# Optimization experiments

Measured on AMD Instinct MI355X. Metric: run time of the kernel, lower is better.

## Reference

```python
import math
import jax, jax.numpy as jnp
import numpy as np

DIM = 2048
N_HEADS = 16
HEAD_DIM = DIM // N_HEADS  # 128
BSZ = 2
SEQLEN = 2048
ROPE_THETA = 500000.0


def _make_freqs(seqlen, head_dim, theta):
    inv = 1.0 / (theta ** (np.arange(0, head_dim, 2, dtype=np.float32) / head_dim))
    t = np.arange(seqlen, dtype=np.float32)
    f = np.outer(t, inv)  # [S, hd//2]
    return jnp.asarray(np.cos(f)), jnp.asarray(np.sin(f))


def setup_inputs() -> dict:
    key = jax.random.key(0)
    kx, kq, kk, kv, ko = jax.random.split(key, 5)
    scale = 0.02
    x = jax.random.normal(kx, (BSZ, SEQLEN, DIM), dtype=jnp.float32)
    wq = jax.random.normal(kq, (DIM, DIM), dtype=jnp.float32) * scale
    wk = jax.random.normal(kk, (DIM, DIM), dtype=jnp.float32) * scale
    wv = jax.random.normal(kv, (DIM, DIM), dtype=jnp.float32) * scale
    wo = jax.random.normal(ko, (DIM, DIM), dtype=jnp.float32) * scale
    freqs_cos, freqs_sin = _make_freqs(SEQLEN, HEAD_DIM, ROPE_THETA)
    # causal additive mask: 0 on/below diag, -inf above
    mask = jnp.triu(jnp.full((SEQLEN, SEQLEN), float('-inf'), dtype=jnp.float32), k=1)
    return {"x": x, "start_pos": 0, "freqs_cos": freqs_cos, "freqs_sin": freqs_sin,
            "mask": mask, "wq": wq, "wk": wk, "wv": wv, "wo": wo}


def _apply_rope(t, cos, sin):
    # t: [B, S, H, hd]; cos/sin: [S, hd//2]
    b, s, h, hd = t.shape
    tr = t.reshape(b, s, h, hd // 2, 2)
    a, bb = tr[..., 0], tr[..., 1]
    c = cos[None, :, None, :]
    sn = sin[None, :, None, :]
    out_r = a * c - bb * sn
    out_i = a * sn + bb * c
    return jnp.stack([out_r, out_i], axis=-1).reshape(b, s, h, hd)


def reference(x, start_pos, freqs_cos, freqs_sin, mask, wq, wk, wv, wo):
    b, s, _ = x.shape
    xq = (x @ wq.T).reshape(b, s, N_HEADS, HEAD_DIM)
    xk = (x @ wk.T).reshape(b, s, N_HEADS, HEAD_DIM)
    xv = (x @ wv.T).reshape(b, s, N_HEADS, HEAD_DIM)
    xq = _apply_rope(xq, freqs_cos, freqs_sin)
    xk = _apply_rope(xk, freqs_cos, freqs_sin)
    # [B, H, S, hd]
    xq = xq.transpose(0, 2, 1, 3)
    xk = xk.transpose(0, 2, 1, 3)
    xv = xv.transpose(0, 2, 1, 3)
    scores = jnp.einsum('bhqd,bhkd->bhqk', xq, xk) / math.sqrt(HEAD_DIM)
    scores = scores + mask[None, None, :, :]
    probs = jax.nn.softmax(scores.astype(jnp.float32), axis=-1).astype(xq.dtype)
    out = jnp.einsum('bhqk,bhkd->bhqd', probs, xv)
    out = out.transpose(0, 2, 1, 3).reshape(b, s, -1)
    return out @ wo.T
```

## Files before the change

kernel.cpp:

```cpp
#include <hip/hip_runtime.h>
#include <stdint.h>

#define DIM 2048
#define SEQ 2048
#define NHEADS 16
#define HDIM 128
#define BSZ 2
#define ROWS (BSZ*SEQ)

typedef uint16_t u16;
typedef __attribute__((ext_vector_type(8))) short bf16x8;
typedef __attribute__((ext_vector_type(4))) float fx4;
typedef __attribute__((ext_vector_type(4))) uint16_t u16x4;

typedef const __attribute__((address_space(1))) uint32_t* gp_t;
typedef __attribute__((address_space(3))) uint32_t* lp_t;
#define GLL16(g, l) __builtin_amdgcn_global_load_lds((gp_t)(g), (lp_t)(l), 16, 0, 0)

__device__ inline u16 f2bf(float f) {
  union { float f; uint32_t u; } v; v.f = f;
  uint32_t u = v.u;
  u += 0x7FFFu + ((u >> 16) & 1u);
  return (u16)(u >> 16);
}
__device__ inline float bf2f(u16 h) {
  union { uint32_t u; float f; } v; v.u = ((uint32_t)h) << 16;
  return v.f;
}

__global__ __launch_bounds__(256) void cvt_kernel(const float* __restrict__ src,
                                                  u16* __restrict__ dst, int n4) {
  int i = blockIdx.x * 256 + threadIdx.x;
  if (i >= n4) return;
  fx4 f = *(const fx4*)(src + (size_t)i * 4);
  u16x4 o;
  o[0] = f2bf(f[0]); o[1] = f2bf(f[1]); o[2] = f2bf(f[2]); o[3] = f2bf(f[3]);
  *(u16x4*)(dst + (size_t)i * 4) = o;
}

__device__ inline void gemm128_core(const u16* __restrict__ A, const u16* __restrict__ B,
                                    u16 (&As)[128][32], u16 (&Bs)[128][32],
                                    fx4 (&acc)[4][4], int M0, int N0) {
  const int tid  = threadIdx.x;
  const int lane = tid & 63;
  const int wave = tid >> 6;
  const int wm = (wave >> 1) * 64;
  const int wn = (wave & 1) * 64;
  const int l16 = lane & 15;
  const int q8  = (lane >> 4) * 8;
#pragma unroll
  for (int tm = 0; tm < 4; ++tm)
#pragma unroll
    for (int tn = 0; tn < 4; ++tn) acc[tm][tn] = fx4{0.f, 0.f, 0.f, 0.f};

  const int wrow = wave * 32;
  const size_t laneA = (size_t)(M0 + wrow + (lane >> 2)) * DIM + (lane & 3) * 8;
  const size_t laneB = (size_t)(N0 + wrow + (lane >> 2)) * DIM + (lane & 3) * 8;

  for (int k0 = 0; k0 < DIM; k0 += 32) {
    __syncthreads();
    GLL16(A + laneA + k0,            &As[wrow][0]);
    GLL16(A + laneA + 16 * DIM + k0, &As[wrow + 16][0]);
    GLL16(B + laneB + k0,            &Bs[wrow][0]);
    GLL16(B + laneB + 16 * DIM + k0, &Bs[wrow + 16][0]);
    __syncthreads();
    bf16x8 af[4], bfr[4];
#pragma unroll
    for (int t = 0; t < 4; ++t) {
      af[t]  = *(const bf16x8*)&As[wm + t * 16 + l16][q8];
      bfr[t] = *(const bf16x8*)&Bs[wn + t * 16 + l16][q8];
    }
#pragma unroll
    for (int tm = 0; tm < 4; ++tm)
#pragma unroll
      for (int tn = 0; tn < 4; ++tn)
        acc[tm][tn] = __builtin_amdgcn_mfma_f32_16x16x32_bf16(af[tm], bfr[tn], acc[tm][tn], 0, 0, 0);
  }
}

__global__ __launch_bounds__(256) void gemm_qkv(const u16* __restrict__ A,
    const u16* __restrict__ B0, const u16* __restrict__ B1, const u16* __restrict__ B2,
    u16* __restrict__ C0, u16* __restrict__ C1, u16* __restrict__ C2) {
  __shared__ __align__(16) u16 As[128][32];
  __shared__ __align__(16) u16 Bs[128][32];
  const u16* B = (blockIdx.z == 0) ? B0 : (blockIdx.z == 1) ? B1 : B2;
  u16* C       = (blockIdx.z == 0) ? C0 : (blockIdx.z == 1) ? C1 : C2;
  const int M0 = blockIdx.y * 128, N0 = blockIdx.x * 128;
  fx4 acc[4][4];
  gemm128_core(A, B, As, Bs, acc, M0, N0);
  const int lane = threadIdx.x & 63, wave = threadIdx.x >> 6;
  const int wm = (wave >> 1) * 64, wn = (wave & 1) * 64;
  const int l16 = lane & 15, quad = lane >> 4;
#pragma unroll
  for (int tm = 0; tm < 4; ++tm)
#pragma unroll
    for (int tn = 0; tn < 4; ++tn)
#pragma unroll
      for (int r = 0; r < 4; ++r) {
        size_t row = (size_t)(M0 + wm + tm * 16 + quad * 4 + r);
        size_t col = (size_t)(N0 + wn + tn * 16 + l16);
        C[row * DIM + col] = f2bf(acc[tm][tn][r]);
      }
}

__global__ __launch_bounds__(256) void gemm_out(const u16* __restrict__ A,
                                                const u16* __restrict__ B,
                                                float* __restrict__ C) {
  __shared__ __align__(16) u16 As[128][32];
  __shared__ __align__(16) u16 Bs[128][32];
  const int M0 = blockIdx.y * 128, N0 = blockIdx.x * 128;
  fx4 acc[4][4];
  gemm128_core(A, B, As, Bs, acc, M0, N0);
  const int lane = threadIdx.x & 63, wave = threadIdx.x >> 6;
  const int wm = (wave >> 1) * 64, wn = (wave & 1) * 64;
  const int l16 = lane & 15, quad = lane >> 4;
#pragma unroll
  for (int tm = 0; tm < 4; ++tm)
#pragma unroll
    for (int tn = 0; tn < 4; ++tn)
#pragma unroll
      for (int r = 0; r < 4; ++r) {
        size_t row = (size_t)(M0 + wm + tm * 16 + quad * 4 + r);
        size_t col = (size_t)(N0 + wn + tn * 16 + l16);
        C[row * DIM + col] = acc[tm][tn][r];
      }
}

__global__ __launch_bounds__(256) void rope_kernel(u16* __restrict__ q, u16* __restrict__ k,
                                                   const float* __restrict__ fcos,
                                                   const float* __restrict__ fsin) {
  int idx = blockIdx.x * 256 + threadIdx.x;
  int t = idx >> 22;
  int p_all = idx & ((1 << 22) - 1);
  u16* ptr = t ? k : q;
  int row = p_all >> 10;
  int r   = p_all & 1023;
  int h   = r >> 6;
  int p   = r & 63;
  int s   = row & (SEQ - 1);
  size_t base = (size_t)row * DIM + h * HDIM + 2 * p;
  float a = bf2f(ptr[base]), b = bf2f(ptr[base + 1]);
  float c = fcos[s * 64 + p], sn = fsin[s * 64 + p];
  ptr[base]     = f2bf(a * c - b * sn);
  ptr[base + 1] = f2bf(a * sn + b * c);
}

__global__ __launch_bounds__(256) void vtrans_kernel(const u16* __restrict__ v,
                                                     u16* __restrict__ vtg) {
  __shared__ __align__(16) u16 T[128][72];
  const int tid = threadIdx.x;
  const int s0 = blockIdx.x * 64;
  const int bh = blockIdx.y;
  const int b = bh >> 4, h = bh & 15;
  const size_t vb = ((size_t)b * SEQ + s0) * DIM + h * HDIM;
#pragma unroll
  for (int i = 0; i < 4; ++i) {
    int c = i * 256 + tid;
    int s = c >> 4;
    int d0 = (c & 15) * 8;
    bf16x8 x = *(const bf16x8*)(v + vb + (size_t)s * DIM + d0);
#pragma unroll
    for (int j = 0; j < 8; ++j) T[d0 + j][s] = (u16)x[j];
  }
  __syncthreads();
  const size_t ob = ((size_t)bh * HDIM) * SEQ + s0;
#pragma unroll
  for (int i = 0; i < 4; ++i) {
    int c = i * 256 + tid;
    int d = c >> 3;
    int s8 = (c & 7) * 8;
    *(bf16x8*)(vtg + ob + (size_t)d * SEQ + s8) = *(const bf16x8*)&T[d][s8];
  }
}

__global__ __launch_bounds__(256) void attn_kernel(const u16* __restrict__ qm,
                                                   const u16* __restrict__ km,
                                                   const u16* __restrict__ vtg,
                                                   u16* __restrict__ ao) {
  __shared__ __align__(16) u16 Ks[64][136];
  __shared__ __align__(16) u16 Vt[128][72];
  __shared__ __align__(16) u16 Ps[4][16][72];
  const int tid = threadIdx.x;
  const int lane = tid & 63, wave = tid >> 6;
  const int l16 = lane & 15, quad = lane >> 4;
  const int bh = blockIdx.x;
  const int qt = (SEQ / 64 - 1) - blockIdx.y;
  const int b = bh >> 4, h = bh & 15;
  const int q0 = qt * 64;
  const size_t brow = (size_t)b * SEQ;
  const int hc = h * HDIM;
  const size_t vbase = (size_t)bh * HDIM * SEQ;

  bf16x8 aq[4];
  {
    size_t qbase = (brow + q0 + wave * 16 + l16) * DIM + hc;
#pragma unroll
    for (int dc = 0; dc < 4; ++dc)
      aq[dc] = *(const bf16x8*)(qm + qbase + dc * 32 + quad * 8);
  }
  fx4 o[8];
#pragma unroll
  for (int i = 0; i < 8; ++i) o[i] = fx4{0.f, 0.f, 0.f, 0.f};
  float mr[4], lr[4];
#pragma unroll
  for (int r = 0; r < 4; ++r) { mr[r] = -3e38f; lr[r] = 0.f; }

  bf16x8 kreg[4], vreg[4];
#pragma unroll
  for (int i = 0; i < 4; ++i) {
    int c = i * 256 + tid;
    kreg[i] = *(const bf16x8*)(km + (brow + (c >> 4)) * DIM + hc + (c & 15) * 8);
    vreg[i] = *(const bf16x8*)(vtg + vbase + (size_t)(c >> 3) * SEQ + (c & 7) * 8);
  }

  for (int kt = 0; kt <= qt; ++kt) {
    __syncthreads();
#pragma unroll
    for (int i = 0; i < 4; ++i) {
      int c = i * 256 + tid;
      *(bf16x8*)&Ks[c >> 4][(c & 15) * 8] = kreg[i];
      *(bf16x8*)&Vt[c >> 3][(c & 7) * 8] = vreg[i];
    }
    __syncthreads();
    if (kt < qt) {
      const int kv1 = (kt + 1) * 64;
#pragma unroll
      for (int i = 0; i < 4; ++i) {
        int c = i * 256 + tid;
        kreg[i] = *(const bf16x8*)(km + (brow + kv1 + (c >> 4)) * DIM + hc + (c & 15) * 8);
        vreg[i] = *(const bf16x8*)(vtg + vbase + (size_t)(c >> 3) * SEQ + kv1 + (c & 7) * 8);
      }
    }
    fx4 s[4];
#pragma unroll
    for (int tn = 0; tn < 4; ++tn) {
      fx4 acc = fx4{0.f, 0.f, 0.f, 0.f};
#pragma unroll
      for (int dc = 0; dc < 4; ++dc) {
        bf16x8 bk = *(const bf16x8*)&Ks[tn * 16 + l16][dc * 32 + quad * 8];
        acc = __builtin_amdgcn_mfma_f32_16x16x32_bf16(aq[dc], bk, acc, 0, 0, 0);
      }
      s[tn] = acc * 0.08838834764831845f;
    }
    if (kt == qt) {
      const int kv0 = kt * 64;
#pragma unroll
      for (int tn = 0; tn < 4; ++tn) {
        int kvpos = kv0 + tn * 16 + l16;
#pragma unroll
        for (int r = 0; r < 4; ++r) {
          int qpos = q0 + wave * 16 + quad * 4 + r;
          if (kvpos > qpos) s[tn][r] = -1e30f;
        }
      }
    }
    float alpha[4];
#pragma unroll
    for (int r = 0; r < 4; ++r) {
      float t = fmaxf(fmaxf(s[0][r], s[1][r]), fmaxf(s[2][r], s[3][r]));
      t = fmaxf(t, __shfl_xor(t, 1));
      t = fmaxf(t, __shfl_xor(t, 2));
      t = fmaxf(t, __shfl_xor(t, 4));
      t = fmaxf(t, __shfl_xor(t, 8));
      float mnew = fmaxf(mr[r], t);
      alpha[r] = __expf(mr[r] - mnew);
      float sm = 0.f;
#pragma unroll
      for (int tn = 0; tn < 4; ++tn) {
        float p = __expf(s[tn][r] - mnew);
        s[tn][r] = p;
        sm += p;
      }
      sm += __shfl_xor(sm, 1);
      sm += __shfl_xor(sm, 2);
      sm += __shfl_xor(sm, 4);
      sm += __shfl_xor(sm, 8);
      lr[r] = lr[r] * alpha[r] + sm;
      mr[r] = mnew;
    }
#pragma unroll
    for (int tn = 0; tn < 4; ++tn)
#pragma unroll
      for (int r = 0; r < 4; ++r)
        Ps[wave][quad * 4 + r][tn * 16 + l16] = f2bf(s[tn][r]);
#pragma unroll
    for (int nt = 0; nt < 8; ++nt) {
      fx4 t = o[nt];
      t[0] *= alpha[0]; t[1] *= alpha[1]; t[2] *= alpha[2]; t[3] *= alpha[3];
      o[nt] = t;
    }
#pragma unroll
    for (int t2 = 0; t2 < 2; ++t2) {
      bf16x8 ap = *(const bf16x8*)&Ps[wave][l16][t2 * 32 + quad * 8];
#pragma unroll
      for (int nt = 0; nt < 8; ++nt) {
        bf16x8 bv = *(const bf16x8*)&Vt[nt * 16 + l16][t2 * 32 + quad * 8];
        o[nt] = __builtin_amdgcn_mfma_f32_16x16x32_bf16(ap, bv, o[nt], 0, 0, 0);
      }
    }
  }
#pragma unroll
  for (int nt = 0; nt < 8; ++nt)
#pragma unroll
    for (int r = 0; r < 4; ++r) {
      float val = o[nt][r] / lr[r];
      size_t row = brow + q0 + wave * 16 + quad * 4 + r;
      ao[row * DIM + hc + nt * 16 + l16] = f2bf(val);
    }
}

extern "C" void kernel_launch(void* const* d_in, const int* in_sizes, int n_in,
                              void* d_out, int out_size, void* d_ws, size_t ws_size,
                              hipStream_t stream) {
  const float* x    = (const float*)d_in[0];
  const float* fcos = (const float*)d_in[2];
  const float* fsin = (const float*)d_in[3];
  const float* wq   = (const float*)d_in[5];
  const float* wk   = (const float*)d_in[6];
  const float* wv   = (const float*)d_in[7];
  const float* wo   = (const float*)d_in[8];
  float* out = (float*)d_out;

  const size_t XN = (size_t)ROWS * DIM;
  const size_t WN = (size_t)DIM * DIM;
  u16* ws  = (u16*)d_ws;
  u16* xb  = ws;
  u16* wqb = xb + XN;
  u16* wkb = wqb + WN;
  u16* wvb = wkb + WN;
  u16* wob = wvb + WN;
  u16* q   = wob + WN;
  u16* k   = q + XN;
  u16* v   = k + XN;
  u16* ao  = v + XN;
  u16* vtg = xb;

  cvt_kernel<<<(int)(XN / 4 / 256), 256, 0, stream>>>(x, xb, (int)(XN / 4));
  cvt_kernel<<<(int)(WN / 4 / 256), 256, 0, stream>>>(wq, wqb, (int)(WN / 4));
  cvt_kernel<<<(int)(WN / 4 / 256), 256, 0, stream>>>(wk, wkb, (int)(WN / 4));
  cvt_kernel<<<(int)(WN / 4 / 256), 256, 0, stream>>>(wv, wvb, (int)(WN / 4));
  cvt_kernel<<<(int)(WN / 4 / 256), 256, 0, stream>>>(wo, wob, (int)(WN / 4));

  gemm_qkv<<<dim3(DIM / 128, ROWS / 128, 3), 256, 0, stream>>>(xb, wqb, wkb, wvb, q, k, v);

  rope_kernel<<<2 * ROWS * 1024 / 256, 256, 0, stream>>>(q, k, fcos, fsin);
  vtrans_kernel<<<dim3(SEQ / 64, BSZ * NHEADS), 256, 0, stream>>>(v, vtg);

  attn_kernel<<<dim3(BSZ * NHEADS, SEQ / 64), 256, 0, stream>>>(q, k, vtg, ao);

  gemm_out<<<dim3(DIM / 128, ROWS / 128), 256, 0, stream>>>(ao, wob, out);
}
```

Baseline: 461.8 us.

## Fuse conversions, fold RoPE into QKV GEMM epilogue, enlarge attention query tile

Result: slower. 483.0 us (+4.6%).

```diff
diff --git a/kernel.cpp b/kernel.cpp
--- a/kernel.cpp
+++ b/kernel.cpp
@@ -28,11 +28,23 @@
   return v.f;
 }
 
-__global__ __launch_bounds__(256) void cvt_kernel(const float* __restrict__ src,
-                                                  u16* __restrict__ dst, int n4) {
+__global__ __launch_bounds__(256) void cvt5_kernel(const float* __restrict__ sx,
+    const float* __restrict__ s1, const float* __restrict__ s2,
+    const float* __restrict__ s3, const float* __restrict__ s4,
+    u16* __restrict__ dst) {
+  const int XC = (ROWS * DIM) / 4;
+  const int WC = (DIM * DIM) / 4;
   int i = blockIdx.x * 256 + threadIdx.x;
-  if (i >= n4) return;
-  fx4 f = *(const fx4*)(src + (size_t)i * 4);
+  const float* src;
+  int off;
+  if (i < XC) { src = sx; off = i; }
+  else {
+    int t = i - XC;
+    int w = t >> 20;
+    off = t & (WC - 1);
+    src = (w == 0) ? s1 : (w == 1) ? s2 : (w == 2) ? s3 : s4;
+  }
+  fx4 f = *(const fx4*)(src + (size_t)off * 4);
   u16x4 o;
   o[0] = f2bf(f[0]); o[1] = f2bf(f[1]); o[2] = f2bf(f[2]); o[3] = f2bf(f[3]);
   *(u16x4*)(dst + (size_t)i * 4) = o;
@@ -80,7 +92,8 @@
 
 __global__ __launch_bounds__(256) void gemm_qkv(const u16* __restrict__ A,
     const u16* __restrict__ B0, const u16* __restrict__ B1, const u16* __restrict__ B2,
-    u16* __restrict__ C0, u16* __restrict__ C1, u16* __restrict__ C2) {
+    u16* __restrict__ C0, u16* __restrict__ C1, u16* __restrict__ C2,
+    const float* __restrict__ fcos, const float* __restrict__ fsin) {
   __shared__ __align__(16) u16 As[128][32];
   __shared__ __align__(16) u16 Bs[128][32];
   const u16* B = (blockIdx.z == 0) ? B0 : (blockIdx.z == 1) ? B1 : B2;
@@ -91,16 +104,39 @@
   const int lane = threadIdx.x & 63, wave = threadIdx.x >> 6;
   const int wm = (wave >> 1) * 64, wn = (wave & 1) * 64;
   const int l16 = lane & 15, quad = lane >> 4;
-#pragma unroll
-  for (int tm = 0; tm < 4; ++tm)
-#pragma unroll
-    for (int tn = 0; tn < 4; ++tn)
-#pragma unroll
-      for (int r = 0; r < 4; ++r) {
-        size_t row = (size_t)(M0 + wm + tm * 16 + quad * 4 + r);
-        size_t col = (size_t)(N0 + wn + tn * 16 + l16);
-        C[row * DIM + col] = f2bf(acc[tm][tn][r]);
-      }
+  if (blockIdx.z < 2) {
+    const bool odd = l16 & 1;
+#pragma unroll
+    for (int tm = 0; tm < 4; ++tm)
+#pragma unroll
+      for (int tn = 0; tn < 4; ++tn) {
+        int col = N0 + wn + tn * 16 + l16;
+        int p = (col & 127) >> 1;
+#pragma unroll
+        for (int r = 0; r < 4; ++r) {
+          int row = M0 + wm + tm * 16 + quad * 4 + r;
+          int s_pos = row & (SEQ - 1);
+          float val = acc[tm][tn][r];
+          float partner = __shfl_xor(val, 1);
+          float c = fcos[s_pos * 64 + p], sn = fsin[s_pos * 64 + p];
+          float a = odd ? partner : val;
+          float bb = odd ? val : partner;
+          float outv = odd ? (a * sn + bb * c) : (a * c - bb * sn);
+          C[(size_t)row * DIM + col] = f2bf(outv);
+        }
+      }
+  } else {
+#pragma unroll
+    for (int tm = 0; tm < 4; ++tm)
+#pragma unroll
+      for (int tn = 0; tn < 4; ++tn)
+#pragma unroll
+        for (int r = 0; r < 4; ++r) {
+          size_t row = (size_t)(M0 + wm + tm * 16 + quad * 4 + r);
+          size_t col = (size_t)(N0 + wn + tn * 16 + l16);
+          C[row * DIM + col] = f2bf(acc[tm][tn][r]);
+        }
+  }
 }
 
 __global__ __launch_bounds__(256) void gemm_out(const u16* __restrict__ A,
@@ -126,25 +162,6 @@
       }
 }
 
-__global__ __launch_bounds__(256) void rope_kernel(u16* __restrict__ q, u16* __restrict__ k,
-                                                   const float* __restrict__ fcos,
-                                                   const float* __restrict__ fsin) {
-  int idx = blockIdx.x * 256 + threadIdx.x;
-  int t = idx >> 22;
-  int p_all = idx & ((1 << 22) - 1);
-  u16* ptr = t ? k : q;
-  int row = p_all >> 10;
-  int r   = p_all & 1023;
-  int h   = r >> 6;
-  int p   = r & 63;
-  int s   = row & (SEQ - 1);
-  size_t base = (size_t)row * DIM + h * HDIM + 2 * p;
-  float a = bf2f(ptr[base]), b = bf2f(ptr[base + 1]);
-  float c = fcos[s * 64 + p], sn = fsin[s * 64 + p];
-  ptr[base]     = f2bf(a * c - b * sn);
-  ptr[base + 1] = f2bf(a * sn + b * c);
-}
-
 __global__ __launch_bounds__(256) void vtrans_kernel(const u16* __restrict__ v,
                                                      u16* __restrict__ vtg) {
   __shared__ __align__(16) u16 T[128][72];
@@ -173,37 +190,43 @@
   }
 }
 
-__global__ __launch_bounds__(256) void attn_kernel(const u16* __restrict__ qm,
-                                                   const u16* __restrict__ km,
-                                                   const u16* __restrict__ vtg,
-                                                   u16* __restrict__ ao) {
+__global__ __launch_bounds__(256, 2) void attn_kernel(const u16* __restrict__ qm,
+                                                      const u16* __restrict__ km,
+                                                      const u16* __restrict__ vtg,
+                                                      u16* __restrict__ ao) {
   __shared__ __align__(16) u16 Ks[64][136];
   __shared__ __align__(16) u16 Vt[128][72];
-  __shared__ __align__(16) u16 Ps[4][16][72];
+  __shared__ __align__(16) u16 Ps[4][32][72];
   const int tid = threadIdx.x;
   const int lane = tid & 63, wave = tid >> 6;
   const int l16 = lane & 15, quad = lane >> 4;
-  const int bh = blockIdx.x;
-  const int qt = (SEQ / 64 - 1) - blockIdx.y;
+  const int idx = blockIdx.x;
+  const int bh = idx & 31;
+  const int j = idx >> 5;
+  const int qt = (j < 8) ? (15 - j) : (j - 8);
   const int b = bh >> 4, h = bh & 15;
-  const int q0 = qt * 64;
+  const int q0 = qt * 128;
   const size_t brow = (size_t)b * SEQ;
   const int hc = h * HDIM;
   const size_t vbase = (size_t)bh * HDIM * SEQ;
-
-  bf16x8 aq[4];
-  {
-    size_t qbase = (brow + q0 + wave * 16 + l16) * DIM + hc;
+  const int nkt = 2 * qt + 2;
+
+  bf16x8 aq[2][4];
+#pragma unroll
+  for (int mt = 0; mt < 2; ++mt) {
+    size_t qbase = (brow + q0 + wave * 32 + mt * 16 + l16) * DIM + hc;
 #pragma unroll
     for (int dc = 0; dc < 4; ++dc)
-      aq[dc] = *(const bf16x8*)(qm + qbase + dc * 32 + quad * 8);
-  }
-  fx4 o[8];
-#pragma unroll
-  for (int i = 0; i < 8; ++i) o[i] = fx4{0.f, 0.f, 0.f, 0.f};
-  float mr[4], lr[4];
-#pragma unroll
-  for (int r = 0; r < 4; ++r) { mr[r] = -3e38f; lr[r] = 0.f; }
+      aq[mt][dc] = *(const bf16x8*)(qm + qbase + dc * 32 + quad * 8);
+  }
+  fx4 o[16];
+#pragma unroll
+  for (int i = 0; i < 16; ++i) o[i] = fx4{0.f, 0.f, 0.f, 0.f};
+  float mr[2][4], lr[2][4];
+#pragma unroll
+  for (int mt = 0; mt < 2; ++mt)
+#pragma unroll
+    for (int r = 0; r < 4; ++r) { mr[mt][r] = -3e38f; lr[mt][r] = 0.f; }
 
   bf16x8 kreg[4], vreg[4];
 #pragma unroll
@@ -213,7 +236,7 @@
     vreg[i] = *(const bf16x8*)(vtg + vbase + (size_t)(c >> 3) * SEQ + (c & 7) * 8);
   }
 
-  for (int kt = 0; kt <= qt; ++kt) {
+  for (int kt = 0; kt < nkt; ++kt) {
     __syncthreads();
 #pragma unroll
     for (int i = 0; i < 4; ++i) {
@@ -222,7 +245,7 @@
       *(bf16x8*)&Vt[c >> 3][(c & 7) * 8] = vreg[i];
     }
     __syncthreads();
-    if (kt < qt) {
+    if (kt + 1 < nkt) {
       const int kv1 = (kt + 1) * 64;
 #pragma unroll
       for (int i = 0; i < 4; ++i) {
@@ -231,82 +254,97 @@
         vreg[i] = *(const bf16x8*)(vtg + vbase + (size_t)(c >> 3) * SEQ + kv1 + (c & 7) * 8);
       }
     }
-    fx4 s[4];
+    fx4 s[2][4];
 #pragma unroll
     for (int tn = 0; tn < 4; ++tn) {
-      fx4 acc = fx4{0.f, 0.f, 0.f, 0.f};
+      fx4 a0 = fx4{0.f, 0.f, 0.f, 0.f}, a1 = fx4{0.f, 0.f, 0.f, 0.f};
 #pragma unroll
       for (int dc = 0; dc < 4; ++dc) {
         bf16x8 bk = *(const bf16x8*)&Ks[tn * 16 + l16][dc * 32 + quad * 8];
-        acc = __builtin_amdgcn_mfma_f32_16x16x32_bf16(aq[dc], bk, acc, 0, 0, 0);
-      }
-      s[tn] = acc * 0.08838834764831845f;
-    }
-    if (kt == qt) {
+        a0 = __builtin_amdgcn_mfma_f32_16x16x32_bf16(aq[0][dc], bk, a0, 0, 0, 0);
+        a1 = __builtin_amdgcn_mfma_f32_16x16x32_bf16(aq[1][dc], bk, a1, 0, 0, 0);
+      }
+      s[0][tn] = a0 * 0.08838834764831845f;
+      s[1][tn] = a1 * 0.08838834764831845f;
+    }
+    if (kt >= nkt - 2) {
       const int kv0 = kt * 64;
 #pragma unroll
-      for (int tn = 0; tn < 4; ++tn) {
-        int kvpos = kv0 + tn * 16 + l16;
-#pragma unroll
-        for (int r = 0; r < 4; ++r) {
-          int qpos = q0 + wave * 16 + quad * 4 + r;
-          if (kvpos > qpos) s[tn][r] = -1e30f;
+      for (int mt = 0; mt < 2; ++mt)
+#pragma unroll
+        for (int tn = 0; tn < 4; ++tn) {
+          int kvpos = kv0 + tn * 16 + l16;
+#pragma unroll
+          for (int r = 0; r < 4; ++r) {
+            int qpos = q0 + wave * 32 + mt * 16 + quad * 4 + r;
+            if (kvpos > qpos) s[mt][tn][r] = -1e30f;
+          }
         }
-      }
-    }
-    float alpha[4];
-#pragma unroll
-    for (int r = 0; r < 4; ++r) {
-      float t = fmaxf(fmaxf(s[0][r], s[1][r]), fmaxf(s[2][r], s[3][r]));
-      t = fmaxf(t, __shfl_xor(t, 1));
-      t = fmaxf(t, __shfl_xor(t, 2));
-      t = fmaxf(t, __shfl_xor(t, 4));
-      t = fmaxf(t, __shfl_xor(t, 8));
-      float mnew = fmaxf(mr[r], t);
-      alpha[r] = __expf(mr[r] - mnew);
-      float sm = 0.f;
-#pragma unroll
-      for (int tn = 0; tn < 4; ++tn) {
-        float p = __expf(s[tn][r] - mnew);
-        s[tn][r] = p;
-        sm += p;
-      }
-      sm += __shfl_xor(sm, 1);
-      sm += __shfl_xor(sm, 2);
-      sm += __shfl_xor(sm, 4);
-      sm += __shfl_xor(sm, 8);
-      lr[r] = lr[r] * alpha[r] + sm;
-      mr[r] = mnew;
-    }
-#pragma unroll
-    for (int tn = 0; tn < 4; ++tn)
-#pragma unroll
-      for (int r = 0; r < 4; ++r)
-        Ps[wave][quad * 4 + r][tn * 16 + l16] = f2bf(s[tn][r]);
-#pragma unroll
-    for (int nt = 0; nt < 8; ++nt) {
-      fx4 t = o[nt];
-      t[0] *= alpha[0]; t[1] *= alpha[1]; t[2] *= alpha[2]; t[3] *= alpha[3];
-      o[nt] = t;
-    }
+    }
+    float alpha[2][4];
+#pragma unroll
+    for (int mt = 0; mt < 2; ++mt)
+#pragma unroll
+      for (int r = 0; r < 4; ++r) {
+        float t = fmaxf(fmaxf(s[mt][0][r], s[mt][1][r]), fmaxf(s[mt][2][r], s[mt][3][r]));
+        t = fmaxf(t, __shfl_xor(t, 1));
+        t = fmaxf(t, __shfl_xor(t, 2));
+        t = fmaxf(t, __shfl_xor(t, 4));
+        t = fmaxf(t, __shfl_xor(t, 8));
+        float mnew = fmaxf(mr[mt][r], t);
+        alpha[mt][r] = __expf(mr[mt][r] - mnew);
+        float sm = 0.f;
+#pragma unroll
+        for (int tn = 0; tn < 4; ++tn) {
+          float p = __expf(s[mt][tn][r] - mnew);
+          s[mt][tn][r] = p;
+          sm += p;
+        }
+        sm += __shfl_xor(sm, 1);
+        sm += __shfl_xor(sm, 2);
+        sm += __shfl_xor(sm, 4);
+        sm += __shfl_xor(sm, 8);
+        lr[mt][r] = lr[mt][r] * alpha[mt][r] + sm;
+        mr[mt][r] = mnew;
+      }
+#pragma unroll
+    for (int mt = 0; mt < 2; ++mt)
+#pragma unroll
+      for (int tn = 0; tn < 4; ++tn)
+#pragma unroll
+        for (int r = 0; r < 4; ++r)
+          Ps[wave][mt * 16 + quad * 4 + r][tn * 16 + l16] = f2bf(s[mt][tn][r]);
+#pragma unroll
+    for (int mt = 0; mt < 2; ++mt)
+#pragma unroll
+      for (int nt = 0; nt < 8; ++nt) {
+        fx4 t = o[mt * 8 + nt];
+        t[0] *= alpha[mt][0]; t[1] *= alpha[mt][1];
+        t[2] *= alpha[mt][2]; t[3] *= alpha[mt][3];
+        o[mt * 8 + nt] = t;
+      }
 #pragma unroll
     for (int t2 = 0; t2 < 2; ++t2) {
-      bf16x8 ap = *(const bf16x8*)&Ps[wave][l16][t2 * 32 + quad * 8];
+      bf16x8 ap0 = *(const bf16x8*)&Ps[wave][l16][t2 * 32 + quad * 8];
+      bf16x8 ap1 = *(const bf16x8*)&Ps[wave][16 + l16][t2 * 32 + quad * 8];
 #pragma unroll
       for (int nt = 0; nt < 8; ++nt) {
         bf16x8 bv = *(const bf16x8*)&Vt[nt * 16 + l16][t2 * 32 + quad * 8];
-        o[nt] = __builtin_amdgcn_mfma_f32_16x16x32_bf16(ap, bv, o[nt], 0, 0, 0);
-      }
-    }
-  }
-#pragma unroll
-  for (int nt = 0; nt < 8; ++nt)
-#pragma unroll
-    for (int r = 0; r < 4; ++r) {
-      float val = o[nt][r] / lr[r];
-      size_t row = brow + q0 + wave * 16 + quad * 4 + r;
-      ao[row * DIM + hc + nt * 16 + l16] = f2bf(val);
-    }
+        o[nt]     = __builtin_amdgcn_mfma_f32_16x16x32_bf16(ap0, bv, o[nt], 0, 0, 0);
+        o[8 + nt] = __builtin_amdgcn_mfma_f32_16x16x32_bf16(ap1, bv, o[8 + nt], 0, 0, 0);
+      }
+    }
+  }
+#pragma unroll
+  for (int mt = 0; mt < 2; ++mt)
+#pragma unroll
+    for (int nt = 0; nt < 8; ++nt)
+#pragma unroll
+      for (int r = 0; r < 4; ++r) {
+        float val = o[mt * 8 + nt][r] / lr[mt][r];
+        size_t row = brow + q0 + wave * 32 + mt * 16 + quad * 4 + r;
+        ao[row * DIM + hc + nt * 16 + l16] = f2bf(val);
+      }
 }
 
 extern "C" void kernel_launch(void* const* d_in, const int* in_sizes, int n_in,
@@ -335,18 +373,15 @@
   u16* ao  = v + XN;
   u16* vtg = xb;
 
-  cvt_kernel<<<(int)(XN / 4 / 256), 256, 0, stream>>>(x, xb, (int)(XN / 4));
-  cvt_kernel<<<(int)(WN / 4 / 256), 256, 0, stream>>>(wq, wqb, (int)(WN / 4));
-  cvt_kernel<<<(int)(WN / 4 / 256), 256, 0, stream>>>(wk, wkb, (int)(WN / 4));
-  cvt_kernel<<<(int)(WN / 4 / 256), 256, 0, stream>>>(wv, wvb, (int)(WN / 4));
-  cvt_kernel<<<(int)(WN / 4 / 256), 256, 0, stream>>>(wo, wob, (int)(WN / 4));
-
-  gemm_qkv<<<dim3(DIM / 128, ROWS / 128, 3), 256, 0, stream>>>(xb, wqb, wkb, wvb, q, k, v);
-
-  rope_kernel<<<2 * ROWS * 1024 / 256, 256, 0, stream>>>(q, k, fcos, fsin);
+  const int total_chunks = (int)((XN + 4 * WN) / 4);
+  cvt5_kernel<<<total_chunks / 256, 256, 0, stream>>>(x, wq, wk, wv, wo, ws);
+
+  gemm_qkv<<<dim3(DIM / 128, ROWS / 128, 3), 256, 0, stream>>>(xb, wqb, wkb, wvb,
+                                                               q, k, v, fcos, fsin);
+
   vtrans_kernel<<<dim3(SEQ / 64, BSZ * NHEADS), 256, 0, stream>>>(v, vtg);
 
-  attn_kernel<<<dim3(BSZ * NHEADS, SEQ / 64), 256, 0, stream>>>(q, k, vtg, ao);
+  attn_kernel<<<dim3(512), 256, 0, stream>>>(q, k, vtg, ao);
 
   gemm_out<<<dim3(DIM / 128, ROWS / 128), 256, 0, stream>>>(ao, wob, out);
 }
```
